# Performance work log

Measured on AMD Instinct MI355X. Metric: run time of the kernel, lower is better.

Reference implementation:

```python
import jax, jax.numpy as jnp
import numpy as np

HEADS = 16
ROPE_BASE = 10000.0


def _rope(x):
    # x: [b, h, n, d]. lucidrains partial rotary: RotaryEmbedding(head_dim//2)
    # rotates only the first rot_dim = d//2 channels, interleaved-pair style.
    d = x.shape[-1]
    rot = d // 2
    inv_freq = 1.0 / (ROPE_BASE ** (jnp.arange(0, rot, 2, dtype=jnp.float32) / rot))  # [rot//2]
    pos = jnp.arange(x.shape[2], dtype=jnp.float32)
    freqs = pos[:, None] * inv_freq[None, :]                  # [n, rot//2]
    cos, sin = jnp.cos(freqs), jnp.sin(freqs)
    xr, xp = x[..., :rot], x[..., rot:]
    x1, x2 = xr[..., 0::2], xr[..., 1::2]                     # interleaved pairs
    o1 = x1 * cos - x2 * sin
    o2 = x2 * cos + x1 * sin
    xr_out = jnp.stack([o1, o2], axis=-1).reshape(xr.shape)   # re-interleave
    return jnp.concatenate([xr_out, xp], axis=-1)


def setup_inputs() -> dict:
    key = jax.random.key(0)
    k0, k1 = jax.random.split(key)
    B, N, D = 2, 2048, 2048
    x = jax.random.normal(k0, (B, N, D), dtype=jnp.float32)
    W_qkv = jax.random.normal(k1, (3 * D, D), dtype=jnp.float32) * (D ** -0.5)
    b_qkv = jnp.zeros((3 * D,), dtype=jnp.float32)
    return {"x": x, "W_qkv": W_qkv, "b_qkv": b_qkv}


def reference(x, W_qkv, b_qkv):
    B, N, D = x.shape
    H = HEADS
    hd = D // H
    qkv = x @ W_qkv.T + b_qkv                                  # [b, n, 3d]
    q, k, v = jnp.split(qkv, 3, axis=-1)
    to_heads = lambda t: t.reshape(B, N, H, hd).transpose(0, 2, 1, 3)  # b h n d
    q, k, v = to_heads(q), to_heads(k), to_heads(v)
    q, k = _rope(q), _rope(k)
    scale = 1.0 / np.sqrt(hd)
    scores = jnp.einsum('bhnd,bhmd->bhnm', q, k) * scale
    causal = jnp.tril(jnp.ones((N, N), dtype=bool))
    scores = jnp.where(causal, scores, -jnp.inf)
    attn = jax.nn.softmax(scores, axis=-1)
    y = jnp.einsum('bhnm,bhmd->bhnd', attn, v)
    return y.transpose(0, 2, 1, 3).reshape(B, N, D)
```

## Files before the change

kernel.cpp:

```cpp
#include <hip/hip_runtime.h>
#include <hip/hip_bf16.h>
#include <math.h>

typedef unsigned short u16;
typedef unsigned int u32;
typedef __attribute__((ext_vector_type(8))) short bf16x8;
typedef __attribute__((ext_vector_type(4))) float f32x4;

#define B_ 2
#define N_ 2048
#define D_ 2048
#define H_ 16
#define HD 128
#define GK 2048

__device__ __forceinline__ u16 f2bf(float f) {
  u32 u = __float_as_uint(f);
  u = (u + 0x7fffu + ((u >> 16) & 1u)) >> 16;
  return (u16)u;
}

__device__ __forceinline__ u32 cvtpk(float lo, float hi) {
  u32 r;
  asm("v_cvt_pk_bf16_f32 %0, %1, %2" : "=v"(r) : "v"(lo), "v"(hi));
  return r;
}

__device__ __forceinline__ void gload_lds16(const void* g, void* l) {
  __builtin_amdgcn_global_load_lds(
      (const __attribute__((address_space(1))) u32*)g,
      (__attribute__((address_space(3))) u32*)l, 16, 0, 0);
}

__global__ __launch_bounds__(256) void cvt_kernel(const float* __restrict__ in,
                                                  u16* __restrict__ out, int n4) {
  int i = blockIdx.x * blockDim.x + threadIdx.x;
  int st = gridDim.x * blockDim.x;
  for (; i < n4; i += st) {
    float4 v = ((const float4*)in)[i];
    ushort4 o;
    o.x = f2bf(v.x); o.y = f2bf(v.y); o.z = f2bf(v.z); o.w = f2bf(v.w);
    ((ushort4*)out)[i] = o;
  }
}

__global__ __launch_bounds__(256) void rope_tbl_kernel(float* __restrict__ tbl) {
  int i = blockIdx.x * blockDim.x + threadIdx.x;
  if (i >= N_ * 32) return;
  int pos = i >> 5, p = i & 31;
  double inv = pow(10000.0, -(double)p / 32.0);
  double a = (double)pos * inv;
  tbl[2 * i]     = (float)cos(a);
  tbl[2 * i + 1] = (float)sin(a);
}

__global__ __launch_bounds__(256) void qkv_gemm_kernel(
    const u16* __restrict__ X, const u16* __restrict__ W,
    const float* __restrict__ bias, const float* __restrict__ tbl,
    u16* __restrict__ Qo, u16* __restrict__ Ko, u16* __restrict__ Vo) {
  __shared__ u16 As[2][128 * 32];
  __shared__ u16 Bs[2][128 * 32];
  const int tid = threadIdx.x;
  const int lane = tid & 63;
  const int w = tid >> 6;
  const int wr = w >> 1, wc = w & 1;
  const int m0 = blockIdx.y * 128;
  const int n0 = blockIdx.x * 128;
  const int l15 = lane & 15, l4 = lane >> 4;

  f32x4 acc[4][4];
#pragma unroll
  for (int a = 0; a < 4; ++a)
#pragma unroll
    for (int b = 0; b < 4; ++b)
#pragma unroll
      for (int q = 0; q < 4; ++q) acc[a][b][q] = 0.f;

  auto stage = [&](int buf, int k0) {
#pragma unroll
    for (int i = 0; i < 4; ++i) {
      int c = w * 4 + i;
      int cc = c & 7;
      int o = cc * 1024 + lane * 16;
      int lo = o ^ (((o >> 7) & 3) << 4);
      int row = lo >> 6;
      int kb2 = (lo & 63) >> 1;
      if (c < 8) {
        gload_lds16(X + (size_t)(m0 + row) * GK + k0 + kb2, As[buf] + cc * 512);
      } else {
        gload_lds16(W + (size_t)(n0 + row) * GK + k0 + kb2, Bs[buf] + cc * 512);
      }
    }
  };

  auto compute = [&](int buf) {
    bf16x8 a[4], b[4];
#pragma unroll
    for (int mf = 0; mf < 4; ++mf) {
      int row = wr * 64 + mf * 16 + l15;
      int off = (row * 64 + l4 * 16) ^ (((row >> 1) & 3) << 4);
      a[mf] = *(const bf16x8*)((const char*)As[buf] + off);
    }
#pragma unroll
    for (int nf = 0; nf < 4; ++nf) {
      int row = wc * 64 + nf * 16 + l15;
      int off = (row * 64 + l4 * 16) ^ (((row >> 1) & 3) << 4);
      b[nf] = *(const bf16x8*)((const char*)Bs[buf] + off);
    }
#pragma unroll
    for (int mf = 0; mf < 4; ++mf)
#pragma unroll
      for (int nf = 0; nf < 4; ++nf)
        acc[mf][nf] = __builtin_amdgcn_mfma_f32_16x16x32_bf16(a[mf], b[nf],
                                                              acc[mf][nf], 0, 0, 0);
  };

  stage(0, 0);
  __syncthreads();
  for (int kt = 0; kt < GK / 32; ++kt) {
    if (kt + 1 < GK / 32) stage((kt + 1) & 1, (kt + 1) * 32);
    compute(kt & 1);
    __syncthreads();
  }

  const float QSCALE = 0.08838834764831845f;
#pragma unroll
  for (int nf = 0; nf < 4; ++nf) {
    int gn = n0 + wc * 64 + nf * 16 + l15;
    float bv = bias[gn];
    int sec = gn >> 11;
    int wi = gn & 2047;
    int h = wi >> 7;
    int d = wi & 127;
    u16* dstbase = (sec == 0) ? Qo : (sec == 1) ? Ko : Vo;
    float mulf = (sec == 0) ? QSCALE : 1.f;
    bool doRope = (sec < 2) && (d < 64);
    int pidx = d >> 1;
    bool odd = (d & 1) != 0;
#pragma unroll
    for (int mf = 0; mf < 4; ++mf) {
#pragma unroll
      for (int j = 0; j < 4; ++j) {
        int gm = m0 + wr * 64 + mf * 16 + l4 * 4 + j;
        int bb = gm >> 11;
        int pos = gm & 2047;
        float v = acc[mf][nf][j] + bv;
        float pr = __shfl_xor(v, 1);
        float ov = v;
        if (doRope) {
          float2 cs = ((const float2*)tbl)[pos * 32 + pidx];
          ov = odd ? (v * cs.x + pr * cs.y) : (v * cs.x - pr * cs.y);
        }
        dstbase[(size_t)((bb * H_ + h) * N_ + pos) * HD + d] = f2bf(ov * mulf);
      }
    }
  }
}

__global__ __launch_bounds__(256, 2) void flash_kernel(
    const u16* __restrict__ Q, const u16* __restrict__ K, const u16* __restrict__ V,
    float* __restrict__ Out) {
  __shared__ char smem[69632];

  const int tid = threadIdx.x, lane = tid & 63, w = tid >> 6;
  const int l15 = lane & 15, l4 = lane >> 4;

  const int bid = blockIdx.x;
  const int xcd = bid & 7, slot = bid >> 3;
  const int bh = xcd * 4 + (slot >> 4);
  const int x = 15 - (slot & 15);
  const int bb = bh >> 4, h = bh & 15;
  const size_t base = (size_t)bh * (N_ * HD);
  const int q0 = x * 128;
  const int nt = 2 * x + 2;

  bf16x8 qf[2][4];
#pragma unroll
  for (int g = 0; g < 2; ++g) {
    const u16* qp = Q + base + (size_t)(q0 + w * 32 + g * 16 + l15) * HD + l4 * 8;
#pragma unroll
    for (int kf = 0; kf < 4; ++kf) qf[g][kf] = *(const bf16x8*)(qp + kf * 32);
  }

  float m_r[2] = {-1e30f, -1e30f}, l_r[2] = {0.f, 0.f};
  f32x4 accO[2][8];
#pragma unroll
  for (int g = 0; g < 2; ++g)
#pragma unroll
    for (int df = 0; df < 8; ++df)
#pragma unroll
      for (int q = 0; q < 4; ++q) accO[g][df][q] = 0.f;

  auto stageK = [&](int buf, int t0) {
    const u16* kb = K + base + (size_t)t0 * HD;
    char* kt = smem + buf * 16384;
#pragma unroll
    for (int i = 0; i < 4; ++i) {
      int c = w * 4 + i;
      int o = c * 1024 + lane * 16;
      int lo = o ^ (((o >> 8) & 7) << 4);
      gload_lds16(kb + (lo >> 1), kt + c * 1024);
    }
  };
  auto loadV = [&](int t0, bf16x8* vr) {
    const u16* vp = V + base + (size_t)(t0 + lane) * HD + w * 32;
#pragma unroll
    for (int i = 0; i < 4; ++i) vr[i] = *(const bf16x8*)(vp + i * 8);
  };
  auto writeV = [&](int buf, const bf16x8* vr) {
    u16* vt = (u16*)(smem + 32768 + buf * 18432);
#pragma unroll
    for (int i = 0; i < 4; ++i)
#pragma unroll
      for (int jj = 0; jj < 8; ++jj)
        vt[(w * 32 + i * 8 + jj) * 72 + lane] = (u16)vr[i][jj];
  };

  const int src0 = l15 + 32 * (l4 & 1);
  const int src1 = src0 + 16;
  const int half = l4 >> 1;
  union U8 { u32 u[4]; bf16x8 v; };

  bf16x8 vreg[4];
  stageK(0, 0);
  loadV(0, vreg);
  writeV(0, vreg);
  __syncthreads();

  for (int t = 0; t < nt; ++t) {
    const int cur = t & 1;
    const int t0 = t * 64;
    const bool pre = (t + 1 < nt);
    if (pre) { stageK(cur ^ 1, t0 + 64); loadV(t0 + 64, vreg); }

    const char* kt = smem + cur * 16384;
    const u16* vt = (const u16*)(smem + 32768 + cur * 18432);

    f32x4 s[2][4];
#pragma unroll
    for (int cf = 0; cf < 4; ++cf) {
#pragma unroll
      for (int q = 0; q < 4; ++q) { s[0][cf][q] = 0.f; s[1][cf][q] = 0.f; }
      int row = cf * 16 + l15;
      int sw = (row & 7) << 4;
#pragma unroll
      for (int kf = 0; kf < 4; ++kf) {
        int off = (row * 256 + kf * 64 + l4 * 16) ^ sw;
        bf16x8 kfrag = *(const bf16x8*)(kt + off);
        s[0][cf] = __builtin_amdgcn_mfma_f32_16x16x32_bf16(kfrag, qf[0][kf], s[0][cf], 0, 0, 0);
        s[1][cf] = __builtin_amdgcn_mfma_f32_16x16x32_bf16(kfrag, qf[1][kf], s[1][cf], 0, 0, 0);
      }
    }

    u32 pk[2][4][2];
#pragma unroll
    for (int g = 0; g < 2; ++g) {
      const int qbase = q0 + w * 32 + g * 16;
      if (t0 + 63 > qbase) {
        const int qg = qbase + l15;
#pragma unroll
        for (int cf = 0; cf < 4; ++cf)
#pragma unroll
          for (int j = 0; j < 4; ++j) {
            int kvg = t0 + cf * 16 + l4 * 4 + j;
            if (kvg > qg) s[g][cf][j] = -1e30f;
          }
      }
      float pmax = s[g][0][0];
#pragma unroll
      for (int cf = 0; cf < 4; ++cf)
#pragma unroll
        for (int j = 0; j < 4; ++j) pmax = fmaxf(pmax, s[g][cf][j]);
      pmax = fmaxf(pmax, __shfl_xor(pmax, 16));
      pmax = fmaxf(pmax, __shfl_xor(pmax, 32));

      if (!__all(pmax <= m_r[g] + 8.f)) {
        float mn = fmaxf(m_r[g], pmax);
        float rs = __expf(m_r[g] - mn);
        m_r[g] = mn;
        l_r[g] *= rs;
#pragma unroll
        for (int df = 0; df < 8; ++df)
#pragma unroll
          for (int j = 0; j < 4; ++j) accO[g][df][j] *= rs;
      }

      float ps = 0.f;
#pragma unroll
      for (int cf = 0; cf < 4; ++cf) {
        float p0 = __expf(s[g][cf][0] - m_r[g]);
        float p1 = __expf(s[g][cf][1] - m_r[g]);
        float p2 = __expf(s[g][cf][2] - m_r[g]);
        float p3 = __expf(s[g][cf][3] - m_r[g]);
        ps += (p0 + p1) + (p2 + p3);
        pk[g][cf][0] = cvtpk(p0, p1);
        pk[g][cf][1] = cvtpk(p2, p3);
      }
      ps += __shfl_xor(ps, 16);
      ps += __shfl_xor(ps, 32);
      l_r[g] += ps;
    }

#pragma unroll
    for (int c = 0; c < 2; ++c) {
      const int c2 = 2 * c;
      U8 pu[2];
#pragma unroll
      for (int g = 0; g < 2; ++g) {
        u32 a0 = (u32)__shfl((int)pk[g][c2][0], src0);
        u32 b0 = (u32)__shfl((int)pk[g][c2 + 1][0], src0);
        u32 a1 = (u32)__shfl((int)pk[g][c2][1], src0);
        u32 b1 = (u32)__shfl((int)pk[g][c2 + 1][1], src0);
        u32 a2 = (u32)__shfl((int)pk[g][c2][0], src1);
        u32 b2 = (u32)__shfl((int)pk[g][c2 + 1][0], src1);
        u32 a3 = (u32)__shfl((int)pk[g][c2][1], src1);
        u32 b3 = (u32)__shfl((int)pk[g][c2 + 1][1], src1);
        pu[g].u[0] = half ? b0 : a0;
        pu[g].u[1] = half ? b1 : a1;
        pu[g].u[2] = half ? b2 : a2;
        pu[g].u[3] = half ? b3 : a3;
      }
#pragma unroll
      for (int df = 0; df < 8; ++df) {
        bf16x8 vf = *(const bf16x8*)(vt + (df * 16 + l15) * 72 + c * 32 + l4 * 8);
        accO[0][df] = __builtin_amdgcn_mfma_f32_16x16x32_bf16(vf, pu[0].v, accO[0][df], 0, 0, 0);
        accO[1][df] = __builtin_amdgcn_mfma_f32_16x16x32_bf16(vf, pu[1].v, accO[1][df], 0, 0, 0);
      }
    }

    if (pre) writeV(cur ^ 1, vreg);
    __syncthreads();
  }

  float* Obuf = (float*)(smem + w * 8448);
  const int l31 = lane & 31;
#pragma unroll
  for (int g = 0; g < 2; ++g) {
    float inv = 1.f / l_r[g];
#pragma unroll
    for (int df = 0; df < 8; ++df) {
      f32x4 v = accO[g][df];
#pragma unroll
      for (int j = 0; j < 4; ++j) v[j] *= inv;
      *(f32x4*)&Obuf[l15 * 132 + df * 16 + l4 * 4] = v;
    }
#pragma unroll
    for (int p = 0; p < 8; ++p) {
      int row = p * 2 + (lane >> 5);
      f32x4 v = *(const f32x4*)&Obuf[row * 132 + l31 * 4];
      int qg = q0 + w * 32 + g * 16 + row;
      *(f32x4*)&Out[(size_t)(bb * N_ + qg) * D_ + h * HD + l31 * 4] = v;
    }
  }
}

extern "C" void kernel_launch(void* const* d_in, const int* in_sizes, int n_in,
                              void* d_out, int out_size, void* d_ws, size_t ws_size,
                              hipStream_t stream) {
  const float* x  = (const float*)d_in[0];
  const float* Wq = (const float*)d_in[1];
  const float* bq = (const float*)d_in[2];
  float* out = (float*)d_out;
  char* ws = (char*)d_ws;

  u16* Qb  = (u16*)(ws);
  u16* Kb  = (u16*)(ws + 16777216);
  u16* Vb  = (u16*)(ws + 2 * 16777216);
  u16* Xb  = (u16*)(ws + 3 * 16777216);
  u16* Wb  = (u16*)(ws + 4 * 16777216);
  float* tbl = (float*)(ws + 4 * 16777216 + 25165824);

  cvt_kernel<<<2048, 256, 0, stream>>>(x, Xb, (B_ * N_ * D_) / 4);
  cvt_kernel<<<2048, 256, 0, stream>>>(Wq, Wb, (3 * D_ * D_) / 4);
  rope_tbl_kernel<<<(N_ * 32 + 255) / 256, 256, 0, stream>>>(tbl);
  qkv_gemm_kernel<<<dim3(48, 32), 256, 0, stream>>>(Xb, Wb, bq, tbl, Qb, Kb, Vb);
  flash_kernel<<<512, 256, 0, stream>>>(Qb, Kb, Vb, out);
}
```

Baseline: 264.7 us.

## Restructure QKV GEMM into 256x192 tiles with 8-wave interleaved pipelined schedule

Rewrites the QKV projection GEMM to use 512-thread blocks computing 256x192 output tiles with K-step 64, a 1D grid swizzled for XCD locality, and a fine-grained schedule. That schedule interleaves LDS reads, async global-to-LDS stages, barriers and MFMA groups under raised wave priority. The aim is to raise arithmetic intensity per tile, cut barrier and load stalls, and overlap memory traffic with MFMA work. In exchange it uses far more LDS and registers, and its correctness depends on manual vmcnt bookkeeping.

```diff
diff --git a/kernel.cpp b/kernel.cpp
--- a/kernel.cpp
+++ b/kernel.cpp
@@ -54,79 +54,141 @@
   tbl[2 * i + 1] = (float)sin(a);
 }
 
-__global__ __launch_bounds__(256) void qkv_gemm_kernel(
+__global__ __launch_bounds__(512, 2) void qkv_gemm_kernel(
     const u16* __restrict__ X, const u16* __restrict__ W,
     const float* __restrict__ bias, const float* __restrict__ tbl,
     u16* __restrict__ Qo, u16* __restrict__ Ko, u16* __restrict__ Vo) {
-  __shared__ u16 As[2][128 * 32];
-  __shared__ u16 Bs[2][128 * 32];
+  __shared__ char smem[114688];
   const int tid = threadIdx.x;
   const int lane = tid & 63;
   const int w = tid >> 6;
-  const int wr = w >> 1, wc = w & 1;
-  const int m0 = blockIdx.y * 128;
-  const int n0 = blockIdx.x * 128;
+  const int wm = w >> 2, wn = w & 3;
   const int l15 = lane & 15, l4 = lane >> 4;
 
-  f32x4 acc[4][4];
-#pragma unroll
-  for (int a = 0; a < 4; ++a)
-#pragma unroll
-    for (int b = 0; b < 4; ++b)
-#pragma unroll
-      for (int q = 0; q < 4; ++q) acc[a][b][q] = 0.f;
-
-  auto stage = [&](int buf, int k0) {
-#pragma unroll
-    for (int i = 0; i < 4; ++i) {
-      int c = w * 4 + i;
-      int cc = c & 7;
-      int o = cc * 1024 + lane * 16;
-      int lo = o ^ (((o >> 7) & 3) << 4);
-      int row = lo >> 6;
-      int kb2 = (lo & 63) >> 1;
-      if (c < 8) {
-        gload_lds16(X + (size_t)(m0 + row) * GK + k0 + kb2, As[buf] + cc * 512);
-      } else {
-        gload_lds16(W + (size_t)(n0 + row) * GK + k0 + kb2, Bs[buf] + cc * 512);
-      }
-    }
-  };
-
-  auto compute = [&](int buf) {
-    bf16x8 a[4], b[4];
-#pragma unroll
-    for (int mf = 0; mf < 4; ++mf) {
-      int row = wr * 64 + mf * 16 + l15;
-      int off = (row * 64 + l4 * 16) ^ (((row >> 1) & 3) << 4);
-      a[mf] = *(const bf16x8*)((const char*)As[buf] + off);
-    }
-#pragma unroll
-    for (int nf = 0; nf < 4; ++nf) {
-      int row = wc * 64 + nf * 16 + l15;
-      int off = (row * 64 + l4 * 16) ^ (((row >> 1) & 3) << 4);
-      b[nf] = *(const bf16x8*)((const char*)Bs[buf] + off);
-    }
-#pragma unroll
-    for (int mf = 0; mf < 4; ++mf)
-#pragma unroll
-      for (int nf = 0; nf < 4; ++nf)
-        acc[mf][nf] = __builtin_amdgcn_mfma_f32_16x16x32_bf16(a[mf], b[nf],
-                                                              acc[mf][nf], 0, 0, 0);
-  };
-
-  stage(0, 0);
-  __syncthreads();
-  for (int kt = 0; kt < GK / 32; ++kt) {
-    if (kt + 1 < GK / 32) stage((kt + 1) & 1, (kt + 1) * 32);
-    compute(kt & 1);
-    __syncthreads();
-  }
+  const int bid = blockIdx.x;
+  const int wg = (bid & 7) * 64 + (bid >> 3);
+  const int n0 = (wg & 31) * 192;
+  const int m0 = (wg >> 5) * 256;
+
+  f32x4 acc[8][3];
+#pragma unroll
+  for (int fm = 0; fm < 8; ++fm)
+#pragma unroll
+    for (int fn = 0; fn < 3; ++fn)
+#pragma unroll
+      for (int q = 0; q < 4; ++q) acc[fm][fn][q] = 0.f;
+
+  auto stageA = [&](int cb, int half, int k0) {
+    char* dst = smem + cb * 57344 + half * 16384;
+    const u16* src = X + (size_t)(m0 + half * 128) * GK + k0;
+#pragma unroll
+    for (int p = 0; p < 2; ++p) {
+      int o = (w * 2 + p) * 1024 + lane * 16;
+      int lo = o ^ (((o >> 7) & 7) << 4);
+      gload_lds16(src + (size_t)(lo >> 7) * GK + ((lo & 127) >> 1),
+                  dst + (w * 2 + p) * 1024);
+    }
+  };
+  auto stageB = [&](int cb, int chunk, int k0) {
+    char* dst = smem + cb * 57344 + 32768 + chunk * 8192;
+    const u16* src = W + (size_t)(n0 + chunk * 64) * GK + k0;
+    int o = w * 1024 + lane * 16;
+    int lo = o ^ (((o >> 7) & 7) << 4);
+    gload_lds16(src + (size_t)(lo >> 7) * GK + ((lo & 127) >> 1), dst + w * 1024);
+  };
+
+  const int NK = GK / 64;
+
+  stageA(0, 0, 0); stageA(0, 1, 0);
+  stageB(0, 0, 0); stageB(0, 1, 0); stageB(0, 2, 0);
+  stageA(1, 0, 64); stageA(1, 1, 64);
+  asm volatile("s_waitcnt vmcnt(4)" ::: "memory");
+  __builtin_amdgcn_s_barrier();
+
+  auto segment = [&](int T, int cb) {
+    const char* Ab = smem + cb * 57344 + wm * 16384;
+    const char* Bb = smem + cb * 57344 + 32768;
+    const int kn1 = (T + 1) * 64, kn2 = (T + 2) * 64;
+    bf16x8 a0[8], a1[8], b0[3], b1[3];
+
+#pragma unroll
+    for (int fm = 0; fm < 8; ++fm) {
+      int r = fm * 16 + l15;
+      a0[fm] = *(const bf16x8*)(Ab + ((r * 128 + l4 * 16) ^ ((r & 7) << 4)));
+    }
+#pragma unroll
+    for (int fn = 0; fn < 3; ++fn) {
+      int r = wn * 48 + fn * 16 + l15;
+      b0[fn] = *(const bf16x8*)(Bb + ((r * 128 + l4 * 16) ^ ((r & 7) << 4)));
+    }
+    if (T + 1 < NK) { stageB(cb ^ 1, 0, kn1); stageB(cb ^ 1, 1, kn1); }
+    __builtin_amdgcn_s_barrier();
+    __builtin_amdgcn_s_setprio(1);
+#pragma unroll
+    for (int fm = 0; fm < 4; ++fm)
+#pragma unroll
+      for (int fn = 0; fn < 3; ++fn)
+        acc[fm][fn] = __builtin_amdgcn_mfma_f32_16x16x32_bf16(a0[fm], b0[fn], acc[fm][fn], 0, 0, 0);
+    __builtin_amdgcn_s_setprio(0);
+    __builtin_amdgcn_s_barrier();
+
+#pragma unroll
+    for (int fm = 0; fm < 8; ++fm) {
+      int r = fm * 16 + l15;
+      a1[fm] = *(const bf16x8*)(Ab + ((r * 128 + 64 + l4 * 16) ^ ((r & 7) << 4)));
+    }
+#pragma unroll
+    for (int fn = 0; fn < 3; ++fn) {
+      int r = wn * 48 + fn * 16 + l15;
+      b1[fn] = *(const bf16x8*)(Bb + ((r * 128 + 64 + l4 * 16) ^ ((r & 7) << 4)));
+    }
+    if (T + 1 < NK) stageB(cb ^ 1, 2, kn1);
+    __builtin_amdgcn_s_barrier();
+    __builtin_amdgcn_s_setprio(1);
+#pragma unroll
+    for (int fm = 4; fm < 8; ++fm)
+#pragma unroll
+      for (int fn = 0; fn < 3; ++fn)
+        acc[fm][fn] = __builtin_amdgcn_mfma_f32_16x16x32_bf16(a0[fm], b0[fn], acc[fm][fn], 0, 0, 0);
+    __builtin_amdgcn_s_setprio(0);
+    __builtin_amdgcn_s_barrier();
+
+    asm volatile("" ::: "memory");
+    if (T + 2 < NK) stageA(cb, 0, kn2);
+    __builtin_amdgcn_s_barrier();
+    __builtin_amdgcn_s_setprio(1);
+#pragma unroll
+    for (int fm = 0; fm < 4; ++fm)
+#pragma unroll
+      for (int fn = 0; fn < 3; ++fn)
+        acc[fm][fn] = __builtin_amdgcn_mfma_f32_16x16x32_bf16(a1[fm], b1[fn], acc[fm][fn], 0, 0, 0);
+    __builtin_amdgcn_s_setprio(0);
+    __builtin_amdgcn_s_barrier();
+
+    asm volatile("" ::: "memory");
+    if (T + 2 < NK) {
+      stageA(cb, 1, kn2);
+      asm volatile("s_waitcnt vmcnt(4)" ::: "memory");
+    } else {
+      asm volatile("s_waitcnt vmcnt(0)" ::: "memory");
+    }
+    __builtin_amdgcn_s_barrier();
+    __builtin_amdgcn_s_setprio(1);
+#pragma unroll
+    for (int fm = 4; fm < 8; ++fm)
+#pragma unroll
+      for (int fn = 0; fn < 3; ++fn)
+        acc[fm][fn] = __builtin_amdgcn_mfma_f32_16x16x32_bf16(a1[fm], b1[fn], acc[fm][fn], 0, 0, 0);
+    __builtin_amdgcn_s_setprio(0);
+    __builtin_amdgcn_s_barrier();
+  };
+
+  for (int T = 0; T < NK; T += 2) { segment(T, 0); segment(T + 1, 1); }
 
   const float QSCALE = 0.08838834764831845f;
 #pragma unroll
-  for (int nf = 0; nf < 4; ++nf) {
-    int gn = n0 + wc * 64 + nf * 16 + l15;
+  for (int fn = 0; fn < 3; ++fn) {
+    int gn = n0 + wn * 48 + fn * 16 + l15;
     float bv = bias[gn];
     int sec = gn >> 11;
     int wi = gn & 2047;
@@ -138,13 +200,13 @@
     int pidx = d >> 1;
     bool odd = (d & 1) != 0;
 #pragma unroll
-    for (int mf = 0; mf < 4; ++mf) {
+    for (int fm = 0; fm < 8; ++fm) {
 #pragma unroll
       for (int j = 0; j < 4; ++j) {
-        int gm = m0 + wr * 64 + mf * 16 + l4 * 4 + j;
+        int gm = m0 + wm * 128 + fm * 16 + l4 * 4 + j;
         int bb = gm >> 11;
         int pos = gm & 2047;
-        float v = acc[mf][nf][j] + bv;
+        float v = acc[fm][fn][j] + bv;
         float pr = __shfl_xor(v, 1);
         float ov = v;
         if (doRope) {
@@ -373,6 +435,6 @@
   cvt_kernel<<<2048, 256, 0, stream>>>(x, Xb, (B_ * N_ * D_) / 4);
   cvt_kernel<<<2048, 256, 0, stream>>>(Wq, Wb, (3 * D_ * D_) / 4);
   rope_tbl_kernel<<<(N_ * 32 + 255) / 256, 256, 0, stream>>>(tbl);
-  qkv_gemm_kernel<<<dim3(48, 32), 256, 0, stream>>>(Xb, Wb, bq, tbl, Qb, Kb, Vb);
+  qkv_gemm_kernel<<<512, 512, 0, stream>>>(Xb, Wb, bq, tbl, Qb, Kb, Vb);
   flash_kernel<<<512, 256, 0, stream>>>(Qb, Kb, Vb, out);
 }
```

New measurement: 255.4 us. 1.04x faster.

## Retile QKV GEMM to 256x384 blocks with 32x32 MFMA and 64-wide K steps

Applied to the files above, without the earlier changes.

Rewrites the QKV projection GEMM to use 512-thread workgroups computing 256x384 output tiles with 32x32x16 bf16 MFMAs, a 64-wide K step, an 8-way XOR LDS swizzle and a remapped grid of 256 blocks. The larger tiles raise arithmetic intensity and cut global traffic and barrier count per FLOP. It also sets MFMA priority and explicit vmcnt waits. The cost is a large 160KB LDS footprint and heavy register use (192 accumulator floats per thread), which limits occupancy to one block per CU. There is also the tail effect of 256 blocks on 256 CUs.

```diff
diff --git a/kernel.cpp b/kernel.cpp
--- a/kernel.cpp
+++ b/kernel.cpp
@@ -6,6 +6,7 @@
 typedef unsigned int u32;
 typedef __attribute__((ext_vector_type(8))) short bf16x8;
 typedef __attribute__((ext_vector_type(4))) float f32x4;
+typedef __attribute__((ext_vector_type(16))) float f32x16;
 
 #define B_ 2
 #define N_ 2048
@@ -54,79 +55,106 @@
   tbl[2 * i + 1] = (float)sin(a);
 }
 
-__global__ __launch_bounds__(256) void qkv_gemm_kernel(
+__global__ __launch_bounds__(512, 2) void qkv_gemm_kernel(
     const u16* __restrict__ X, const u16* __restrict__ W,
     const float* __restrict__ bias, const float* __restrict__ tbl,
     u16* __restrict__ Qo, u16* __restrict__ Ko, u16* __restrict__ Vo) {
-  __shared__ u16 As[2][128 * 32];
-  __shared__ u16 Bs[2][128 * 32];
+  __shared__ char smem[163840];
   const int tid = threadIdx.x;
   const int lane = tid & 63;
   const int w = tid >> 6;
-  const int wr = w >> 1, wc = w & 1;
-  const int m0 = blockIdx.y * 128;
-  const int n0 = blockIdx.x * 128;
-  const int l15 = lane & 15, l4 = lane >> 4;
-
-  f32x4 acc[4][4];
-#pragma unroll
-  for (int a = 0; a < 4; ++a)
-#pragma unroll
-    for (int b = 0; b < 4; ++b)
-#pragma unroll
-      for (int q = 0; q < 4; ++q) acc[a][b][q] = 0.f;
-
-  auto stage = [&](int buf, int k0) {
-#pragma unroll
-    for (int i = 0; i < 4; ++i) {
-      int c = w * 4 + i;
-      int cc = c & 7;
-      int o = cc * 1024 + lane * 16;
-      int lo = o ^ (((o >> 7) & 3) << 4);
-      int row = lo >> 6;
-      int kb2 = (lo & 63) >> 1;
-      if (c < 8) {
-        gload_lds16(X + (size_t)(m0 + row) * GK + k0 + kb2, As[buf] + cc * 512);
-      } else {
-        gload_lds16(W + (size_t)(n0 + row) * GK + k0 + kb2, Bs[buf] + cc * 512);
-      }
-    }
+  const int wm = w >> 2, wn = w & 3;
+  const int l31 = lane & 31, l1 = lane >> 5;
+  const int s16v = l1 * 16;
+
+  const int bid = blockIdx.x;
+  const int wg = (bid & 7) * 32 + (bid >> 3);
+  const int m0 = (wg & 15) * 256;
+  const int n0 = (wg >> 4) * 384;
+
+  int soA[4], soB[6];
+#pragma unroll
+  for (int c = 0; c < 4; ++c) {
+    int o = c * 8192 + tid * 16;
+    int lo = o ^ (((o >> 7) & 7) << 4);
+    soA[c] = (lo >> 7) * GK + ((lo & 127) >> 1);
+  }
+#pragma unroll
+  for (int c = 0; c < 6; ++c) {
+    int o = c * 8192 + tid * 16;
+    int lo = o ^ (((o >> 7) & 7) << 4);
+    soB[c] = (lo >> 7) * GK + ((lo & 127) >> 1);
+  }
+
+  f32x16 acc[4][3];
+#pragma unroll
+  for (int mb = 0; mb < 4; ++mb)
+#pragma unroll
+    for (int nb = 0; nb < 3; ++nb)
+#pragma unroll
+      for (int q = 0; q < 16; ++q) acc[mb][nb][q] = 0.f;
+
+  const u16* Xb = X + (size_t)m0 * GK;
+  const u16* Wb = W + (size_t)n0 * GK;
+
+  auto stageA = [&](char* Ab, int k0) {
+#pragma unroll
+    for (int c = 0; c < 4; ++c)
+      gload_lds16(Xb + soA[c] + k0, Ab + c * 8192 + w * 1024);
   };
-
-  auto compute = [&](int buf) {
-    bf16x8 a[4], b[4];
-#pragma unroll
-    for (int mf = 0; mf < 4; ++mf) {
-      int row = wr * 64 + mf * 16 + l15;
-      int off = (row * 64 + l4 * 16) ^ (((row >> 1) & 3) << 4);
-      a[mf] = *(const bf16x8*)((const char*)As[buf] + off);
-    }
-#pragma unroll
-    for (int nf = 0; nf < 4; ++nf) {
-      int row = wc * 64 + nf * 16 + l15;
-      int off = (row * 64 + l4 * 16) ^ (((row >> 1) & 3) << 4);
-      b[nf] = *(const bf16x8*)((const char*)Bs[buf] + off);
-    }
-#pragma unroll
-    for (int mf = 0; mf < 4; ++mf)
-#pragma unroll
-      for (int nf = 0; nf < 4; ++nf)
-        acc[mf][nf] = __builtin_amdgcn_mfma_f32_16x16x32_bf16(a[mf], b[nf],
-                                                              acc[mf][nf], 0, 0, 0);
+  auto stageB = [&](char* Bb, int k0) {
+#pragma unroll
+    for (int c = 0; c < 6; ++c)
+      gload_lds16(Wb + soB[c] + k0, Bb + c * 8192 + w * 1024);
   };
 
-  stage(0, 0);
-  __syncthreads();
-  for (int kt = 0; kt < GK / 32; ++kt) {
-    if (kt + 1 < GK / 32) stage((kt + 1) & 1, (kt + 1) * 32);
-    compute(kt & 1);
-    __syncthreads();
+  const int NK = GK / 64;
+
+  stageA(smem, 0);
+  stageB(smem + 65536, 0);
+  asm volatile("s_waitcnt vmcnt(0)" ::: "memory");
+  __builtin_amdgcn_s_barrier();
+
+  for (int T = 0; T < NK; ++T) {
+    const int cb = T & 1;
+    const char* Ab = smem + cb * 32768;
+    const char* Bb = smem + 65536 + cb * 49152;
+    if (T + 1 < NK) {
+      stageA(smem + (cb ^ 1) * 32768, (T + 1) * 64);
+      stageB(smem + 65536 + (cb ^ 1) * 49152, (T + 1) * 64);
+    }
+
+#pragma unroll
+    for (int ks = 0; ks < 4; ++ks) {
+      const int inner = ks * 32 + s16v;
+      bf16x8 a[4], b[3];
+#pragma unroll
+      for (int mb = 0; mb < 4; ++mb) {
+        int r = wm * 128 + mb * 32 + l31;
+        a[mb] = *(const bf16x8*)(Ab + r * 128 + (inner ^ ((r & 7) << 4)));
+      }
+#pragma unroll
+      for (int nb = 0; nb < 3; ++nb) {
+        int r = wn * 96 + nb * 32 + l31;
+        b[nb] = *(const bf16x8*)(Bb + r * 128 + (inner ^ ((r & 7) << 4)));
+      }
+      __builtin_amdgcn_s_setprio(1);
+#pragma unroll
+      for (int mb = 0; mb < 4; ++mb)
+#pragma unroll
+        for (int nb = 0; nb < 3; ++nb)
+          acc[mb][nb] = __builtin_amdgcn_mfma_f32_32x32x16_bf16(a[mb], b[nb], acc[mb][nb], 0, 0, 0);
+      __builtin_amdgcn_s_setprio(0);
+    }
+
+    asm volatile("s_waitcnt vmcnt(0)" ::: "memory");
+    __builtin_amdgcn_s_barrier();
   }
 
   const float QSCALE = 0.08838834764831845f;
 #pragma unroll
-  for (int nf = 0; nf < 4; ++nf) {
-    int gn = n0 + wc * 64 + nf * 16 + l15;
+  for (int nb = 0; nb < 3; ++nb) {
+    int gn = n0 + wn * 96 + nb * 32 + l31;
     float bv = bias[gn];
     int sec = gn >> 11;
     int wi = gn & 2047;
@@ -138,13 +166,13 @@
     int pidx = d >> 1;
     bool odd = (d & 1) != 0;
 #pragma unroll
-    for (int mf = 0; mf < 4; ++mf) {
-#pragma unroll
-      for (int j = 0; j < 4; ++j) {
-        int gm = m0 + wr * 64 + mf * 16 + l4 * 4 + j;
+    for (int mb = 0; mb < 4; ++mb) {
+#pragma unroll
+      for (int r = 0; r < 16; ++r) {
+        int gm = m0 + wm * 128 + mb * 32 + (r & 3) + 8 * (r >> 2) + 4 * l1;
         int bb = gm >> 11;
         int pos = gm & 2047;
-        float v = acc[mf][nf][j] + bv;
+        float v = acc[mb][nb][r] + bv;
         float pr = __shfl_xor(v, 1);
         float ov = v;
         if (doRope) {
@@ -373,6 +401,6 @@
   cvt_kernel<<<2048, 256, 0, stream>>>(x, Xb, (B_ * N_ * D_) / 4);
   cvt_kernel<<<2048, 256, 0, stream>>>(Wq, Wb, (3 * D_ * D_) / 4);
   rope_tbl_kernel<<<(N_ * 32 + 255) / 256, 256, 0, stream>>>(tbl);
-  qkv_gemm_kernel<<<dim3(48, 32), 256, 0, stream>>>(Xb, Wb, bq, tbl, Qb, Kb, Vb);
+  qkv_gemm_kernel<<<256, 512, 0, stream>>>(Xb, Wb, bq, tbl, Qb, Kb, Vb);
   flash_kernel<<<512, 256, 0, stream>>>(Qb, Kb, Vb, out);
 }
```

After: 256.7 us. 1.03x faster.
